# Optimization experiments

Measured on AMD Instinct MI355X. Metric: run time of the kernel, lower is better.

The kernel has to match this reference:

```python
import jax, jax.numpy as jnp
import numpy as np

L = 1024  # seq_len


def setup_inputs() -> dict:
    key = jax.random.key(0)
    ks = jax.random.split(key, 9)
    B = 4
    x = jax.random.uniform(ks[0], (B, L, L), dtype=jnp.float32)          # scores from pre_model
    M = (jax.random.uniform(ks[1], (B, L, L)) < 0.5).astype(jnp.float32)  # pairing-constraint mask
    M = M * M.transpose(0, 2, 1)  # symmetric binary mask
    return {
        "x": x,
        "M": M,
        "s": jnp.float32(0.5),
        "w": jax.random.uniform(ks[2], (1,), dtype=jnp.float32),
        "rho_p": jax.random.uniform(ks[3], (L, L), dtype=jnp.float32),
        "alpha": jnp.float32(0.005),
        "belt": jnp.float32(0.05),
        "lr_alpha": jnp.float32(0.99),
        "lr_belt": jnp.float32(0.99),
        "steps": 16,
    }


def _T_A(A_hat, M):
    # symmetrize then mask
    return (A_hat + A_hat.transpose(0, 2, 1)) * 0.5 * M


def reference(x, M, s, w, rho_p, alpha, belt, lr_alpha, lr_belt, steps):
    scores = x                      # pre_model output, [B, L, L]
    U = scores - s
    A_hat0 = scores
    A0 = _T_A(A_hat0, M)
    Lm0 = w * jax.nn.relu(jnp.sum(A0, axis=-1) - 1.0)   # [B, L] (w broadcasts)

    def step(carry, t):
        Lm, A, A_hat = carry
        # G = U/2 - Lm * sign(rowsum(A) - 1), broadcast over last dim
        row = jnp.sum(A, axis=-1) - 1.0                  # [B, L]
        G = U * 0.5 - (Lm * jnp.sign(row))[:, :, None]   # [B, L, L]
        at = alpha * jnp.power(lr_alpha, t)
        A_hat = A_hat + at * A_hat * M * (G + G.transpose(0, 2, 1))
        A_hat = jax.nn.relu(jnp.abs(A_hat) - rho_p * at)  # soft threshold
        A_hat = 1.0 - jax.nn.relu(1.0 - A_hat)            # clip above at 1
        A = _T_A(A_hat, M)
        Lm = Lm + belt * jnp.power(lr_belt, t) * jax.nn.relu(jnp.sum(A, axis=-1) - 1.0)
        return (Lm, A, A_hat), None

    ts = jnp.arange(steps, dtype=jnp.float32)
    (Lm, A, A_hat), _ = jax.lax.scan(step, (Lm0, A0, A_hat0), ts)
    return A
```

## Files before the change

### kernel.cpp

```cpp
#include <hip/hip_runtime.h>
#include <cstddef>
#include <math.h>

static constexpr int L = 1024;
static constexpr int B = 4;
static constexpr int NSTEPS = 16;
static constexpr int NTILE = 16;
static constexpr int NPAIR = NTILE * (NTILE + 1) / 2;

static constexpr size_t AH_OFF  = 0;
static constexpr size_t US_OFF  = (size_t)B * L * L;
static constexpr size_t CP_OFF  = 2 * (size_t)B * L * L;
static constexpr size_t RP0_OFF = CP_OFF + (size_t)B * 256 * L;
static constexpr size_t CP0_OFF = RP0_OFF + (size_t)B * 16 * L;
static constexpr size_t R_OFF   = CP0_OFF + (size_t)B * 16 * L;
static constexpr size_t LM_OFF  = R_OFF + (size_t)B * L;
static constexpr size_t CC_OFF  = LM_OFF + (size_t)B * L;
static constexpr size_t SC_OFF  = CC_OFF + (size_t)B * L;


__global__ __launch_bounds__(256) void init_kernel(
    const float* __restrict__ x, const float* __restrict__ M,
    const float* __restrict__ sp,
    float* __restrict__ ah, float* __restrict__ us,
    float* __restrict__ Rpart, float* __restrict__ Cpart0)
{
    __shared__ float lt[64][65];
    __shared__ float cpw[4][64];
    const int bid  = blockIdx.x;
    const int chunk = bid & 7;
    const int rest  = bid >> 3;
    const int b  = rest >> 5;
    const int ti = (chunk << 1) | ((rest >> 4) & 1);
    const int tj = rest & 15;
    const int t  = threadIdx.x;
    const int w  = t >> 6;
    const int r  = t >> 4;
    const int c4 = (t & 15) << 2;
    const float s = sp[0];
    const float* xb = x + (size_t)b * L * L;

#pragma unroll
    for (int it = 0; it < 4; ++it) {
        int rr = r + 16 * it;
        float4 v = *(const float4*)(xb + (size_t)(tj * 64 + rr) * L + ti * 64 + c4);
        lt[rr][c4+0] = v.x; lt[rr][c4+1] = v.y; lt[rr][c4+2] = v.z; lt[rr][c4+3] = v.w;
    }
    __syncthreads();

    float cs0 = 0.f, cs1 = 0.f, cs2 = 0.f, cs3 = 0.f;
#pragma unroll
    for (int it = 0; it < 4; ++it) {
        int rr = r + 16 * it;
        int gi = ti * 64 + rr;
        size_t off = (size_t)b * L * L + (size_t)gi * L + tj * 64 + c4;
        float4 xv = *(const float4*)(x + off);
        float4 mv = *(const float4*)(M + off);
        *(float4*)(us + off) = make_float4(0.5f*(xv.x + lt[c4+0][rr]) - s,
                                           0.5f*(xv.y + lt[c4+1][rr]) - s,
                                           0.5f*(xv.z + lt[c4+2][rr]) - s,
                                           0.5f*(xv.w + lt[c4+3][rr]) - s);
        float a0 = xv.x*mv.x, a1 = xv.y*mv.y, a2 = xv.z*mv.z, a3 = xv.w*mv.w;
        *(float4*)(ah + off) = make_float4(a0, a1, a2, a3);
        float rs = (a0 + a1) + (a2 + a3);
        rs += __shfl_xor(rs, 1); rs += __shfl_xor(rs, 2);
        rs += __shfl_xor(rs, 4); rs += __shfl_xor(rs, 8);
        if ((t & 15) == 0) Rpart[((size_t)(b * 16 + tj)) * L + gi] = rs;
        cs0 += a0; cs1 += a1; cs2 += a2; cs3 += a3;
    }
    cs0 += __shfl_xor(cs0, 16); cs0 += __shfl_xor(cs0, 32);
    cs1 += __shfl_xor(cs1, 16); cs1 += __shfl_xor(cs1, 32);
    cs2 += __shfl_xor(cs2, 16); cs2 += __shfl_xor(cs2, 32);
    cs3 += __shfl_xor(cs3, 16); cs3 += __shfl_xor(cs3, 32);
    if ((t & 63) < 16) {
        int c0 = (t & 63) << 2;
        cpw[w][c0+0] = cs0; cpw[w][c0+1] = cs1; cpw[w][c0+2] = cs2; cpw[w][c0+3] = cs3;
    }
    __syncthreads();
    if (t < 64)
        Cpart0[((size_t)(b * 16 + ti)) * L + tj * 64 + t] =
            (cpw[0][t] + cpw[1][t]) + (cpw[2][t] + cpw[3][t]);
}

__global__ __launch_bounds__(256) void lminit_kernel(
    const float* __restrict__ wp,
    const float* __restrict__ alphap, const float* __restrict__ beltp,
    const float* __restrict__ lrap,  const float* __restrict__ lrbp,
    const float* __restrict__ Rpart, const float* __restrict__ Cpart0,
    float* __restrict__ Lm, float* __restrict__ cc, float* __restrict__ sc)
{
    const int bid = blockIdx.x;
    const int t   = threadIdx.x;
    if (bid == 0 && t < NSTEPS) {
        sc[t]          = alphap[0] * powf(lrap[0], (float)t);
        sc[NSTEPS + t] = beltp[0]  * powf(lrbp[0], (float)t);
    }
    const int b   = bid >> 2;
    const int i   = ((bid & 3) << 8) + t;
    float R0 = 0.f, C0 = 0.f;
#pragma unroll
    for (int k = 0; k < 16; ++k) {
        R0 += Rpart[((size_t)(b * 16 + k)) * L + i];
        C0 += Cpart0[((size_t)(b * 16 + k)) * L + i];
    }
    float rowv = 0.5f * (R0 + C0) - 1.0f;
    float rl = fmaxf(rowv, 0.f);
    float lm = wp[0] * rl;
    Lm[b * L + i] = lm;
    float sg = (rowv > 0.f) ? 1.f : ((rowv < 0.f) ? -1.f : 0.f);
    cc[b * L + i] = lm * sg;
}

__device__ __forceinline__ float step_elem(float a, float u, float rho,
                                           float ci, float cj, float at) {
    float g = u - ci - cj;
    float v = a * (1.f + at * g);
    v = fmaxf(fabsf(v) - rho * at, 0.f);
    return fminf(v, 1.f);
}

__global__ __launch_bounds__(512) void update_kernel(
    const float* __restrict__ rho, const float* __restrict__ sc,
    float* __restrict__ ah, const float* __restrict__ us,
    const float* __restrict__ cc,
    float* __restrict__ R, float* __restrict__ Cpart, int p)
{
    __shared__ float cp[8][1024];
    const int bid   = blockIdx.x;
    const int chunk = bid & 7;
    const int rest  = bid >> 3;
    const int b     = rest >> 4;
    const int slab  = (chunk << 4) | (rest & 15);
    const int t    = threadIdx.x;
    const int w    = t >> 6;
    const int l    = t & 63;
    const int row  = (slab << 3) + w;
    const size_t rowoff = (size_t)b * L * L + (size_t)row * L;
    const float at = sc[p];
    const float* ccb = cc + b * L;

    float4 cj[4];
#pragma unroll
    for (int k = 0; k < 4; ++k)
        cj[k] = *(const float4*)(ccb + k * 256 + l * 4);
    const float ci = ccb[row];

    float4 a4[4], u4[4], h4[4];
#pragma unroll
    for (int k = 0; k < 4; ++k) {
        const size_t off = rowoff + k * 256 + l * 4;
        a4[k] = *(const float4*)(ah + off);
        u4[k] = *(const float4*)(us + off);
        h4[k] = *(const float4*)(rho + (size_t)row * L + k * 256 + l * 4);
    }
#pragma unroll
    for (int k = 0; k < 4; ++k) {
        a4[k].x = step_elem(a4[k].x, u4[k].x, h4[k].x, ci, cj[k].x, at);
        a4[k].y = step_elem(a4[k].y, u4[k].y, h4[k].y, ci, cj[k].y, at);
        a4[k].z = step_elem(a4[k].z, u4[k].z, h4[k].z, ci, cj[k].z, at);
        a4[k].w = step_elem(a4[k].w, u4[k].w, h4[k].w, ci, cj[k].w, at);
        *(float4*)(ah + rowoff + k * 256 + l * 4) = a4[k];
    }

    float rs = 0.f;
#pragma unroll
    for (int k = 0; k < 4; ++k)
        rs += (a4[k].x + a4[k].y) + (a4[k].z + a4[k].w);
    rs += __shfl_xor(rs, 1);  rs += __shfl_xor(rs, 2);  rs += __shfl_xor(rs, 4);
    rs += __shfl_xor(rs, 8);  rs += __shfl_xor(rs, 16); rs += __shfl_xor(rs, 32);
    if (l == 0) R[b * L + row] = rs;

#pragma unroll
    for (int k = 0; k < 4; ++k)
        *(float4*)&cp[w][k * 256 + l * 4] = a4[k];
    __syncthreads();
    const int c0 = t * 2;
    float2 acc = make_float2(0.f, 0.f);
#pragma unroll
    for (int j = 0; j < 8; ++j) {
        float2 v = *(float2*)&cp[j][c0];
        acc.x += v.x; acc.y += v.y;
    }
    *(float2*)(Cpart + ((size_t)(b * 128 + slab)) * L + c0) = acc;
}

__global__ __launch_bounds__(1024) void lmreduce_kernel(
    const float* __restrict__ sc,
    const float* __restrict__ Cpart, const float* __restrict__ R,
    float* __restrict__ Lm, float* __restrict__ cc, int p)
{
    __shared__ float red[16][64];
    const int bid = blockIdx.x;
    const int b   = bid >> 4;
    const int c0  = (bid & 15) << 6;
    const int t   = threadIdx.x;
    const int w   = t >> 6;
    const int l   = t & 63;
    const int c   = c0 + l;

    const float* base = Cpart + (size_t)b * 128 * L + c;
    float v = 0.f;
#pragma unroll
    for (int k = w * 8; k < w * 8 + 8; ++k)
        v += base[(size_t)k * L];
    red[w][l] = v;
    __syncthreads();

    if (w == 0) {
        float total = 0.f;
#pragma unroll
        for (int j = 0; j < 16; ++j) total += red[j][l];
        float rowv = 0.5f * (R[b * L + c] + total) - 1.0f;
        float rl = fmaxf(rowv, 0.f);
        float lm = Lm[b * L + c] + sc[NSTEPS + p] * rl;
        Lm[b * L + c] = lm;
        float sg = (rowv > 0.f) ? 1.f : ((rowv < 0.f) ? -1.f : 0.f);
        cc[b * L + c] = lm * sg;
    }
}

__device__ __forceinline__ void decode_pair(int p, int& ti, int& tj) {
    int t = 0;
    while (p >= NTILE - t) { p -= NTILE - t; ++t; }
    ti = t; tj = t + p;
}

__global__ __launch_bounds__(256) void updfinal_kernel(
    const float* __restrict__ rho, const float* __restrict__ sc,
    const float* __restrict__ ah, const float* __restrict__ us,
    const float* __restrict__ cc, float* __restrict__ out)
{
    __shared__ float la[64][65];
    __shared__ float lb[64][65];
    __shared__ float uu[64][65];
    const int task = blockIdx.x;
    const int b = task / NPAIR;
    int ti, tj; decode_pair(task % NPAIR, ti, tj);
    const int t  = threadIdx.x;
    const int r0 = t >> 4;
    const int c0 = (t & 15) << 2;
    const float at = sc[NSTEPS - 1];
    const float* ccb = cc + b * L;
    const float* ahb = ah  + (size_t)b * L * L;
    const float* usb = us  + (size_t)b * L * L;
    float* ob        = out + (size_t)b * L * L;

    {
        float4 cjv = *(const float4*)(ccb + tj * 64 + c0);
        for (int it = 0; it < 4; ++it) {
            int r = r0 + 16 * it;
            int gi = ti * 64 + r;
            size_t off = (size_t)gi * L + tj * 64 + c0;
            float4 av = *(const float4*)(ahb + off);
            float4 uv = *(const float4*)(usb + off);
            float4 hv = *(const float4*)(rho + off);
            float ci = ccb[gi];
            la[r][c0+0] = step_elem(av.x, uv.x, hv.x, ci, cjv.x, at);
            la[r][c0+1] = step_elem(av.y, uv.y, hv.y, ci, cjv.y, at);
            la[r][c0+2] = step_elem(av.z, uv.z, hv.z, ci, cjv.z, at);
            la[r][c0+3] = step_elem(av.w, uv.w, hv.w, ci, cjv.w, at);
            uu[r][c0+0] = uv.x; uu[r][c0+1] = uv.y;
            uu[r][c0+2] = uv.z; uu[r][c0+3] = uv.w;
        }
    }
    __syncthreads();
    if (ti != tj) {
        float4 cjv = *(const float4*)(ccb + ti * 64 + c0);
        for (int it = 0; it < 4; ++it) {
            int r = r0 + 16 * it;
            int gi = tj * 64 + r;
            size_t off = (size_t)gi * L + ti * 64 + c0;
            float4 av = *(const float4*)(ahb + off);
            float4 hv = *(const float4*)(rho + off);
            float ci = ccb[gi];
            lb[r][c0+0] = step_elem(av.x, uu[c0+0][r], hv.x, ci, cjv.x, at);
            lb[r][c0+1] = step_elem(av.y, uu[c0+1][r], hv.y, ci, cjv.y, at);
            lb[r][c0+2] = step_elem(av.z, uu[c0+2][r], hv.z, ci, cjv.z, at);
            lb[r][c0+3] = step_elem(av.w, uu[c0+3][r], hv.w, ci, cjv.w, at);
        }
    }
    __syncthreads();

    for (int it = 0; it < 4; ++it) {
        int r = r0 + 16 * it;
        size_t off = (size_t)(ti * 64 + r) * L + tj * 64 + c0;
        float tb0, tb1, tb2, tb3;
        if (ti == tj) { tb0 = la[c0+0][r]; tb1 = la[c0+1][r]; tb2 = la[c0+2][r]; tb3 = la[c0+3][r]; }
        else          { tb0 = lb[c0+0][r]; tb1 = lb[c0+1][r]; tb2 = lb[c0+2][r]; tb3 = lb[c0+3][r]; }
        *(float4*)(ob + off) = make_float4(0.5f*(la[r][c0+0]+tb0), 0.5f*(la[r][c0+1]+tb1),
                                           0.5f*(la[r][c0+2]+tb2), 0.5f*(la[r][c0+3]+tb3));
    }
    if (ti != tj) {
        for (int it = 0; it < 4; ++it) {
            int r = r0 + 16 * it;
            size_t off = (size_t)(tj * 64 + r) * L + ti * 64 + c0;
            *(float4*)(ob + off) = make_float4(0.5f*(lb[r][c0+0]+la[c0+0][r]),
                                               0.5f*(lb[r][c0+1]+la[c0+1][r]),
                                               0.5f*(lb[r][c0+2]+la[c0+2][r]),
                                               0.5f*(lb[r][c0+3]+la[c0+3][r]));
        }
    }
}

extern "C" void kernel_launch(void* const* d_in, const int* in_sizes, int n_in,
                              void* d_out, int out_size, void* d_ws, size_t ws_size,
                              hipStream_t stream) {
    const float* x     = (const float*)d_in[0];
    const float* M     = (const float*)d_in[1];
    const float* s     = (const float*)d_in[2];
    const float* w     = (const float*)d_in[3];
    const float* rho   = (const float*)d_in[4];
    const float* alpha = (const float*)d_in[5];
    const float* belt  = (const float*)d_in[6];
    const float* lra   = (const float*)d_in[7];
    const float* lrb   = (const float*)d_in[8];
    float* out = (float*)d_out;

    float* ws     = (float*)d_ws;
    float* ah     = ws + AH_OFF;
    float* us     = ws + US_OFF;
    float* Cpart  = ws + CP_OFF;
    float* Rpart  = ws + RP0_OFF;
    float* Cpart0 = ws + CP0_OFF;
    float* R      = ws + R_OFF;
    float* Lm     = ws + LM_OFF;
    float* cc     = ws + CC_OFF;
    float* sc     = ws + SC_OFF;

    init_kernel<<<dim3(1024), dim3(256), 0, stream>>>(x, M, s, ah, us, Rpart, Cpart0);
    lminit_kernel<<<dim3(16), dim3(256), 0, stream>>>(
        w, alpha, belt, lra, lrb, Rpart, Cpart0, Lm, cc, sc);
    for (int p = 0; p < NSTEPS - 1; ++p) {
        update_kernel<<<dim3(512), dim3(512), 0, stream>>>(
            rho, sc, ah, us, cc, R, Cpart, p);
        lmreduce_kernel<<<dim3(64), dim3(1024), 0, stream>>>(
            sc, Cpart, R, Lm, cc, p);
    }
    updfinal_kernel<<<dim3(B * NPAIR), dim3(256), 0, stream>>>(
        rho, sc, ah, us, cc, out);
}
```

Baseline: 273.8 us.

## Process mirrored tile pairs per block to reuse symmetric U and shrink partial reductions

Replaces the row-slab update kernel with one that handles a (ti,tj) tile and its mirror (tj,ti) in the same block. The U tile is loaded once and its transpose, staged in shared memory, serves the mirrored tile, which roughly halves U traffic per step. Row and column partial sums are now produced per 64-wide tile, so the per-step reduction kernel reads 16 partials per element instead of 128 and runs as a small 16-block launch. In exchange, diagonal-tile blocks do half the work of the others, the mirrored tile reads U through transposed shared-memory access, and the block adds extra synchronisation points.

```diff
diff --git a/kernel.cpp b/kernel.cpp
--- a/kernel.cpp
+++ b/kernel.cpp
@@ -7,23 +7,22 @@
 static constexpr int NSTEPS = 16;
 static constexpr int NTILE = 16;
 static constexpr int NPAIR = NTILE * (NTILE + 1) / 2;
+static constexpr int BL = B * L;
 
 static constexpr size_t AH_OFF  = 0;
 static constexpr size_t US_OFF  = (size_t)B * L * L;
-static constexpr size_t CP_OFF  = 2 * (size_t)B * L * L;
-static constexpr size_t RP0_OFF = CP_OFF + (size_t)B * 256 * L;
-static constexpr size_t CP0_OFF = RP0_OFF + (size_t)B * 16 * L;
-static constexpr size_t R_OFF   = CP0_OFF + (size_t)B * 16 * L;
-static constexpr size_t LM_OFF  = R_OFF + (size_t)B * L;
-static constexpr size_t CC_OFF  = LM_OFF + (size_t)B * L;
-static constexpr size_t SC_OFF  = CC_OFF + (size_t)B * L;
+static constexpr size_t RP_OFF  = 2 * (size_t)B * L * L;
+static constexpr size_t CP_OFF  = RP_OFF + (size_t)B * 16 * L;
+static constexpr size_t LM_OFF  = CP_OFF + (size_t)B * 16 * L;
+static constexpr size_t CC_OFF  = LM_OFF + (size_t)BL;
+static constexpr size_t SC_OFF  = CC_OFF + (size_t)BL;
 
 
 __global__ __launch_bounds__(256) void init_kernel(
     const float* __restrict__ x, const float* __restrict__ M,
     const float* __restrict__ sp,
     float* __restrict__ ah, float* __restrict__ us,
-    float* __restrict__ Rpart, float* __restrict__ Cpart0)
+    float* __restrict__ Rpart, float* __restrict__ Cpart)
 {
     __shared__ float lt[64][65];
     __shared__ float cpw[4][64];
@@ -78,7 +77,7 @@
     }
     __syncthreads();
     if (t < 64)
-        Cpart0[((size_t)(b * 16 + ti)) * L + tj * 64 + t] =
+        Cpart[((size_t)(b * 16 + ti)) * L + tj * 64 + t] =
             (cpw[0][t] + cpw[1][t]) + (cpw[2][t] + cpw[3][t]);
 }
 
@@ -86,7 +85,7 @@
     const float* __restrict__ wp,
     const float* __restrict__ alphap, const float* __restrict__ beltp,
     const float* __restrict__ lrap,  const float* __restrict__ lrbp,
-    const float* __restrict__ Rpart, const float* __restrict__ Cpart0,
+    const float* __restrict__ Rpart, const float* __restrict__ Cpart,
     float* __restrict__ Lm, float* __restrict__ cc, float* __restrict__ sc)
 {
     const int bid = blockIdx.x;
@@ -101,7 +100,7 @@
 #pragma unroll
     for (int k = 0; k < 16; ++k) {
         R0 += Rpart[((size_t)(b * 16 + k)) * L + i];
-        C0 += Cpart0[((size_t)(b * 16 + k)) * L + i];
+        C0 += Cpart[((size_t)(b * 16 + k)) * L + i];
     }
     float rowv = 0.5f * (R0 + C0) - 1.0f;
     float rl = fmaxf(rowv, 0.f);
@@ -119,110 +118,136 @@
     return fminf(v, 1.f);
 }
 
-__global__ __launch_bounds__(512) void update_kernel(
-    const float* __restrict__ rho, const float* __restrict__ sc,
-    float* __restrict__ ah, const float* __restrict__ us,
-    const float* __restrict__ cc,
-    float* __restrict__ R, float* __restrict__ Cpart, int p)
-{
-    __shared__ float cp[8][1024];
-    const int bid   = blockIdx.x;
-    const int chunk = bid & 7;
-    const int rest  = bid >> 3;
-    const int b     = rest >> 4;
-    const int slab  = (chunk << 4) | (rest & 15);
-    const int t    = threadIdx.x;
-    const int w    = t >> 6;
-    const int l    = t & 63;
-    const int row  = (slab << 3) + w;
-    const size_t rowoff = (size_t)b * L * L + (size_t)row * L;
-    const float at = sc[p];
-    const float* ccb = cc + b * L;
-
-    float4 cj[4];
-#pragma unroll
-    for (int k = 0; k < 4; ++k)
-        cj[k] = *(const float4*)(ccb + k * 256 + l * 4);
-    const float ci = ccb[row];
-
-    float4 a4[4], u4[4], h4[4];
-#pragma unroll
-    for (int k = 0; k < 4; ++k) {
-        const size_t off = rowoff + k * 256 + l * 4;
-        a4[k] = *(const float4*)(ah + off);
-        u4[k] = *(const float4*)(us + off);
-        h4[k] = *(const float4*)(rho + (size_t)row * L + k * 256 + l * 4);
-    }
-#pragma unroll
-    for (int k = 0; k < 4; ++k) {
-        a4[k].x = step_elem(a4[k].x, u4[k].x, h4[k].x, ci, cj[k].x, at);
-        a4[k].y = step_elem(a4[k].y, u4[k].y, h4[k].y, ci, cj[k].y, at);
-        a4[k].z = step_elem(a4[k].z, u4[k].z, h4[k].z, ci, cj[k].z, at);
-        a4[k].w = step_elem(a4[k].w, u4[k].w, h4[k].w, ci, cj[k].w, at);
-        *(float4*)(ah + rowoff + k * 256 + l * 4) = a4[k];
-    }
-
-    float rs = 0.f;
-#pragma unroll
-    for (int k = 0; k < 4; ++k)
-        rs += (a4[k].x + a4[k].y) + (a4[k].z + a4[k].w);
-    rs += __shfl_xor(rs, 1);  rs += __shfl_xor(rs, 2);  rs += __shfl_xor(rs, 4);
-    rs += __shfl_xor(rs, 8);  rs += __shfl_xor(rs, 16); rs += __shfl_xor(rs, 32);
-    if (l == 0) R[b * L + row] = rs;
-
-#pragma unroll
-    for (int k = 0; k < 4; ++k)
-        *(float4*)&cp[w][k * 256 + l * 4] = a4[k];
-    __syncthreads();
-    const int c0 = t * 2;
-    float2 acc = make_float2(0.f, 0.f);
-#pragma unroll
-    for (int j = 0; j < 8; ++j) {
-        float2 v = *(float2*)&cp[j][c0];
-        acc.x += v.x; acc.y += v.y;
-    }
-    *(float2*)(Cpart + ((size_t)(b * 128 + slab)) * L + c0) = acc;
-}
-
-__global__ __launch_bounds__(1024) void lmreduce_kernel(
-    const float* __restrict__ sc,
-    const float* __restrict__ Cpart, const float* __restrict__ R,
-    float* __restrict__ Lm, float* __restrict__ cc, int p)
-{
-    __shared__ float red[16][64];
-    const int bid = blockIdx.x;
-    const int b   = bid >> 4;
-    const int c0  = (bid & 15) << 6;
-    const int t   = threadIdx.x;
-    const int w   = t >> 6;
-    const int l   = t & 63;
-    const int c   = c0 + l;
-
-    const float* base = Cpart + (size_t)b * 128 * L + c;
-    float v = 0.f;
-#pragma unroll
-    for (int k = w * 8; k < w * 8 + 8; ++k)
-        v += base[(size_t)k * L];
-    red[w][l] = v;
-    __syncthreads();
-
-    if (w == 0) {
-        float total = 0.f;
-#pragma unroll
-        for (int j = 0; j < 16; ++j) total += red[j][l];
-        float rowv = 0.5f * (R[b * L + c] + total) - 1.0f;
-        float rl = fmaxf(rowv, 0.f);
-        float lm = Lm[b * L + c] + sc[NSTEPS + p] * rl;
-        Lm[b * L + c] = lm;
-        float sg = (rowv > 0.f) ? 1.f : ((rowv < 0.f) ? -1.f : 0.f);
-        cc[b * L + c] = lm * sg;
-    }
-}
-
 __device__ __forceinline__ void decode_pair(int p, int& ti, int& tj) {
     int t = 0;
     while (p >= NTILE - t) { p -= NTILE - t; ++t; }
     ti = t; tj = t + p;
+}
+
+__global__ __launch_bounds__(512) void updpair_kernel(
+    const float* __restrict__ rho, const float* __restrict__ sc,
+    float* __restrict__ ah, const float* __restrict__ us,
+    const float* __restrict__ cc,
+    float* __restrict__ Rpart, float* __restrict__ Cpart, int p)
+{
+    __shared__ float uu[64][65];
+    __shared__ float cpw[8][64];
+    const int task = blockIdx.x;
+    const int b = task / NPAIR;
+    int ti, tj; decode_pair(task % NPAIR, ti, tj);
+    const int t  = threadIdx.x;
+    const int w  = t >> 6;
+    const int r0 = t >> 4;
+    const int c4 = (t & 15) << 2;
+    const float at = sc[p];
+    const float* ccb = cc + b * L;
+    const size_t bb = (size_t)b * L * L;
+
+    {
+        float4 cjv = *(const float4*)(ccb + tj * 64 + c4);
+        float cs0 = 0.f, cs1 = 0.f, cs2 = 0.f, cs3 = 0.f;
+#pragma unroll
+        for (int it = 0; it < 2; ++it) {
+            int r  = r0 + 32 * it;
+            int gi = ti * 64 + r;
+            size_t off = bb + (size_t)gi * L + tj * 64 + c4;
+            float4 av = *(const float4*)(ah + off);
+            float4 uv = *(const float4*)(us + off);
+            float4 hv = *(const float4*)(rho + (size_t)gi * L + tj * 64 + c4);
+            float ci = ccb[gi];
+            float n0 = step_elem(av.x, uv.x, hv.x, ci, cjv.x, at);
+            float n1 = step_elem(av.y, uv.y, hv.y, ci, cjv.y, at);
+            float n2 = step_elem(av.z, uv.z, hv.z, ci, cjv.z, at);
+            float n3 = step_elem(av.w, uv.w, hv.w, ci, cjv.w, at);
+            *(float4*)(ah + off) = make_float4(n0, n1, n2, n3);
+            uu[r][c4+0] = uv.x; uu[r][c4+1] = uv.y;
+            uu[r][c4+2] = uv.z; uu[r][c4+3] = uv.w;
+            float rs = (n0 + n1) + (n2 + n3);
+            rs += __shfl_xor(rs, 1); rs += __shfl_xor(rs, 2);
+            rs += __shfl_xor(rs, 4); rs += __shfl_xor(rs, 8);
+            if ((t & 15) == 0) Rpart[((size_t)(b * 16 + tj)) * L + gi] = rs;
+            cs0 += n0; cs1 += n1; cs2 += n2; cs3 += n3;
+        }
+        cs0 += __shfl_xor(cs0, 16); cs0 += __shfl_xor(cs0, 32);
+        cs1 += __shfl_xor(cs1, 16); cs1 += __shfl_xor(cs1, 32);
+        cs2 += __shfl_xor(cs2, 16); cs2 += __shfl_xor(cs2, 32);
+        cs3 += __shfl_xor(cs3, 16); cs3 += __shfl_xor(cs3, 32);
+        if ((t & 63) < 16) {
+            int c0 = (t & 63) << 2;
+            cpw[w][c0+0] = cs0; cpw[w][c0+1] = cs1;
+            cpw[w][c0+2] = cs2; cpw[w][c0+3] = cs3;
+        }
+    }
+    __syncthreads();
+    if (t < 64) {
+        float tot = 0.f;
+#pragma unroll
+        for (int j = 0; j < 8; ++j) tot += cpw[j][t];
+        Cpart[((size_t)(b * 16 + ti)) * L + tj * 64 + t] = tot;
+    }
+
+    if (ti != tj) {
+        float4 cjv = *(const float4*)(ccb + ti * 64 + c4);
+        float cs0 = 0.f, cs1 = 0.f, cs2 = 0.f, cs3 = 0.f;
+#pragma unroll
+        for (int it = 0; it < 2; ++it) {
+            int r  = r0 + 32 * it;
+            int gi = tj * 64 + r;
+            size_t off = bb + (size_t)gi * L + ti * 64 + c4;
+            float4 av = *(const float4*)(ah + off);
+            float4 hv = *(const float4*)(rho + (size_t)gi * L + ti * 64 + c4);
+            float ci = ccb[gi];
+            float n0 = step_elem(av.x, uu[c4+0][r], hv.x, ci, cjv.x, at);
+            float n1 = step_elem(av.y, uu[c4+1][r], hv.y, ci, cjv.y, at);
+            float n2 = step_elem(av.z, uu[c4+2][r], hv.z, ci, cjv.z, at);
+            float n3 = step_elem(av.w, uu[c4+3][r], hv.w, ci, cjv.w, at);
+            *(float4*)(ah + off) = make_float4(n0, n1, n2, n3);
+            float rs = (n0 + n1) + (n2 + n3);
+            rs += __shfl_xor(rs, 1); rs += __shfl_xor(rs, 2);
+            rs += __shfl_xor(rs, 4); rs += __shfl_xor(rs, 8);
+            if ((t & 15) == 0) Rpart[((size_t)(b * 16 + ti)) * L + gi] = rs;
+            cs0 += n0; cs1 += n1; cs2 += n2; cs3 += n3;
+        }
+        cs0 += __shfl_xor(cs0, 16); cs0 += __shfl_xor(cs0, 32);
+        cs1 += __shfl_xor(cs1, 16); cs1 += __shfl_xor(cs1, 32);
+        cs2 += __shfl_xor(cs2, 16); cs2 += __shfl_xor(cs2, 32);
+        cs3 += __shfl_xor(cs3, 16); cs3 += __shfl_xor(cs3, 32);
+        __syncthreads();
+        if ((t & 63) < 16) {
+            int c0 = (t & 63) << 2;
+            cpw[w][c0+0] = cs0; cpw[w][c0+1] = cs1;
+            cpw[w][c0+2] = cs2; cpw[w][c0+3] = cs3;
+        }
+        __syncthreads();
+        if (t < 64) {
+            float tot = 0.f;
+#pragma unroll
+            for (int j = 0; j < 8; ++j) tot += cpw[j][t];
+            Cpart[((size_t)(b * 16 + tj)) * L + ti * 64 + t] = tot;
+        }
+    }
+}
+
+__global__ __launch_bounds__(256) void lmreduce_kernel(
+    const float* __restrict__ sc,
+    const float* __restrict__ Rpart, const float* __restrict__ Cpart,
+    float* __restrict__ Lm, float* __restrict__ cc, int p)
+{
+    const int bid = blockIdx.x;
+    const int t   = threadIdx.x;
+    const int b   = bid >> 2;
+    const int i   = ((bid & 3) << 8) + t;
+    float R0 = 0.f, C0 = 0.f;
+#pragma unroll
+    for (int k = 0; k < 16; ++k) {
+        R0 += Rpart[((size_t)(b * 16 + k)) * L + i];
+        C0 += Cpart[((size_t)(b * 16 + k)) * L + i];
+    }
+    float rowv = 0.5f * (R0 + C0) - 1.0f;
+    float lm = Lm[b * L + i] + sc[NSTEPS + p] * fmaxf(rowv, 0.f);
+    Lm[b * L + i] = lm;
+    float sg = (rowv > 0.f) ? 1.f : ((rowv < 0.f) ? -1.f : 0.f);
+    cc[b * L + i] = lm * sg;
 }
 
 __global__ __launch_bounds__(256) void updfinal_kernel(
@@ -319,22 +344,20 @@
     float* ws     = (float*)d_ws;
     float* ah     = ws + AH_OFF;
     float* us     = ws + US_OFF;
+    float* Rpart  = ws + RP_OFF;
     float* Cpart  = ws + CP_OFF;
-    float* Rpart  = ws + RP0_OFF;
-    float* Cpart0 = ws + CP0_OFF;
-    float* R      = ws + R_OFF;
     float* Lm     = ws + LM_OFF;
     float* cc     = ws + CC_OFF;
     float* sc     = ws + SC_OFF;
 
-    init_kernel<<<dim3(1024), dim3(256), 0, stream>>>(x, M, s, ah, us, Rpart, Cpart0);
+    init_kernel<<<dim3(1024), dim3(256), 0, stream>>>(x, M, s, ah, us, Rpart, Cpart);
     lminit_kernel<<<dim3(16), dim3(256), 0, stream>>>(
-        w, alpha, belt, lra, lrb, Rpart, Cpart0, Lm, cc, sc);
+        w, alpha, belt, lra, lrb, Rpart, Cpart, Lm, cc, sc);
     for (int p = 0; p < NSTEPS - 1; ++p) {
-        update_kernel<<<dim3(512), dim3(512), 0, stream>>>(
-            rho, sc, ah, us, cc, R, Cpart, p);
-        lmreduce_kernel<<<dim3(64), dim3(1024), 0, stream>>>(
-            sc, Cpart, R, Lm, cc, p);
+        updpair_kernel<<<dim3(B * NPAIR), dim3(512), 0, stream>>>(
+            rho, sc, ah, us, cc, Rpart, Cpart, p);
+        lmreduce_kernel<<<dim3(16), dim3(256), 0, stream>>>(
+            sc, Rpart, Cpart, Lm, cc, p);
     }
     updfinal_kernel<<<dim3(B * NPAIR), dim3(256), 0, stream>>>(
         rho, sc, ah, us, cc, out);
```

New measurement: 314.4 us. +14.8%, slower.
